# Performance work log

Measured on AMD Instinct MI355X. Metric: run time of the kernel, lower is better.

Reference implementation:

```python
import jax, jax.numpy as jnp
import numpy as np

D_MODEL = 512
NUM_HEADS = 8
D_K = D_MODEL // NUM_HEADS


def setup_inputs() -> dict:
    key = jax.random.key(0)
    ks = jax.random.split(key, 9)
    B, N = 4, 2048
    x = jax.random.normal(ks[0], (B, N, D_MODEL), dtype=jnp.float32)
    s = 1.0 / np.sqrt(D_MODEL)
    Wq = jax.random.normal(ks[1], (D_MODEL, D_MODEL), dtype=jnp.float32) * s
    bq = jax.random.normal(ks[2], (D_MODEL,), dtype=jnp.float32) * 0.02
    Wk = jax.random.normal(ks[3], (D_MODEL, D_MODEL), dtype=jnp.float32) * s
    bk = jax.random.normal(ks[4], (D_MODEL,), dtype=jnp.float32) * 0.02
    Wv = jax.random.normal(ks[5], (D_MODEL, D_MODEL), dtype=jnp.float32) * s
    bv = jax.random.normal(ks[6], (D_MODEL,), dtype=jnp.float32) * 0.02
    Wo = jax.random.normal(ks[7], (D_MODEL, D_MODEL), dtype=jnp.float32) * s
    bo = jax.random.normal(ks[8], (D_MODEL,), dtype=jnp.float32) * 0.02
    return {"x": x, "Wq": Wq, "bq": bq, "Wk": Wk, "bk": bk,
            "Wv": Wv, "bv": bv, "Wo": Wo, "bo": bo}


def reference(x, Wq, bq, Wk, bk, Wv, bv, Wo, bo):
    B, N, _ = x.shape
    # project and split heads: [B, H, N, d_k]
    def split_heads(t):
        return t.reshape(B, N, NUM_HEADS, D_K).transpose(0, 2, 1, 3)
    Q = split_heads(x @ Wq + bq)
    K = split_heads(x @ Wk + bk)
    V = split_heads(x @ Wv + bv)
    scale = 1.0 / np.sqrt(D_K)
    scores = jnp.einsum('bhqd,bhkd->bhqk', Q, K) * scale  # [B,H,N,N]
    probs = jax.nn.softmax(scores, axis=-1)
    attn = jnp.einsum('bhqk,bhkd->bhqd', probs, V)
    attn = attn.transpose(0, 2, 1, 3).reshape(B, N, D_MODEL)
    return attn @ Wo + bo
```

## Files before the change

kernel.cpp:

```cpp
#include <hip/hip_runtime.h>
#include <math.h>

#define D_MODEL 512
#define N_SEQ   2048
#define H       8
#define DK      64

typedef __attribute__((ext_vector_type(8))) short bf16x8;
typedef __attribute__((ext_vector_type(4))) float f32x4;

__device__ __forceinline__ unsigned short f2b(float f) {
    unsigned int u = __float_as_uint(f);
    u += 0x7FFF + ((u >> 16) & 1);
    return (unsigned short)(u >> 16);
}

__global__ void convert_bf16(const float* __restrict__ in,
                             unsigned short* __restrict__ out)
{
    const int i = (blockIdx.x * 256 + threadIdx.x) * 8;
    float4 a = *(const float4*)(in + i);
    float4 b = *(const float4*)(in + i + 4);
    ushort4 o0, o1;
    o0.x = f2b(a.x); o0.y = f2b(a.y); o0.z = f2b(a.z); o0.w = f2b(a.w);
    o1.x = f2b(b.x); o1.y = f2b(b.y); o1.z = f2b(b.z); o1.w = f2b(b.w);
    *(ushort4*)(out + i)     = o0;
    *(ushort4*)(out + i + 4) = o1;
}

__global__ void transpose_all(
    const float* __restrict__ W0, const float* __restrict__ W1,
    const float* __restrict__ W2, const float* __restrict__ W3,
    unsigned short* __restrict__ T0, unsigned short* __restrict__ T1,
    unsigned short* __restrict__ T2, unsigned short* __restrict__ T3)
{
    const float* W; unsigned short* Wt;
    if      (blockIdx.z == 0) { W = W0; Wt = T0; }
    else if (blockIdx.z == 1) { W = W1; Wt = T1; }
    else if (blockIdx.z == 2) { W = W2; Wt = T2; }
    else                      { W = W3; Wt = T3; }

    __shared__ float t[32][33];
    const int tx = threadIdx.x, ty = threadIdx.y;
    const int x = blockIdx.x * 32 + tx;
    const int y0 = blockIdx.y * 32;
    for (int i = ty; i < 32; i += 8)
        t[i][tx] = W[(size_t)(y0 + i) * D_MODEL + x];
    __syncthreads();
    const int ox = blockIdx.y * 32 + tx;
    const int oy0 = blockIdx.x * 32;
    for (int i = ty; i < 32; i += 8)
        Wt[(size_t)(oy0 + i) * D_MODEL + ox] = f2b(t[tx][i]);
}

__device__ __forceinline__ void gemm_body(
    const unsigned short* __restrict__ A,
    const unsigned short* __restrict__ Wt,
    const float* __restrict__ bias,
    void* __restrict__ out, int mode, int bx, int by)
{
    __shared__ unsigned short As[128][72];
    __shared__ unsigned short Bs[128][72];

    const int tid  = threadIdx.x;
    const int lane = tid & 63, wave = tid >> 6;
    const int m0 = by * 128, n0 = bx * 128;
    const int wm = (wave & 1) * 64, wn = (wave >> 1) * 64;
    const int cn = lane & 15, g = lane >> 4;

    const int srow = tid >> 1;
    const int scol = (tid & 1) * 32;
    const unsigned short* Ag = A  + (size_t)(m0 + srow) * D_MODEL + scol;
    const unsigned short* Bg = Wt + (size_t)(n0 + srow) * D_MODEL + scol;

    f32x4 acc[4][4];
    #pragma unroll
    for (int i = 0; i < 4; ++i)
        #pragma unroll
        for (int j = 0; j < 4; ++j)
            acc[i][j] = (f32x4){0.f, 0.f, 0.f, 0.f};

    for (int k0 = 0; k0 < D_MODEL; k0 += 64) {
        bf16x8 av[4], bv[4];
        #pragma unroll
        for (int q = 0; q < 4; ++q) {
            av[q] = *(const bf16x8*)(Ag + k0 + q * 8);
            bv[q] = *(const bf16x8*)(Bg + k0 + q * 8);
        }
        __syncthreads();
        #pragma unroll
        for (int q = 0; q < 4; ++q) {
            *(bf16x8*)&As[srow][scol + q * 8] = av[q];
            *(bf16x8*)&Bs[srow][scol + q * 8] = bv[q];
        }
        __syncthreads();

        #pragma unroll
        for (int ks = 0; ks < 2; ++ks) {
            bf16x8 af[4], bf[4];
            #pragma unroll
            for (int i = 0; i < 4; ++i)
                af[i] = *(const bf16x8*)&As[wm + i * 16 + cn][ks * 32 + g * 8];
            #pragma unroll
            for (int j = 0; j < 4; ++j)
                bf[j] = *(const bf16x8*)&Bs[wn + j * 16 + cn][ks * 32 + g * 8];
            #pragma unroll
            for (int i = 0; i < 4; ++i)
                #pragma unroll
                for (int j = 0; j < 4; ++j)
                    acc[i][j] = __builtin_amdgcn_mfma_f32_16x16x32_bf16(
                        af[i], bf[j], acc[i][j], 0, 0, 0);
        }
    }

    if (mode == 2) {
        float* o = (float*)out;
        #pragma unroll
        for (int j = 0; j < 4; ++j) {
            const int n = n0 + wn + j * 16 + cn;
            const float bb = bias[n];
            #pragma unroll
            for (int i = 0; i < 4; ++i)
                #pragma unroll
                for (int r = 0; r < 4; ++r) {
                    const int m = m0 + wm + i * 16 + g * 4 + r;
                    o[(size_t)m * D_MODEL + n] = acc[i][j][r] + bb;
                }
        }
    } else if (mode == 0) {
        unsigned short* o = (unsigned short*)out;
        #pragma unroll
        for (int j = 0; j < 4; ++j) {
            const int n = n0 + wn + j * 16 + cn;
            const int h = n >> 6, d = n & 63;
            const float bb = bias[n];
            #pragma unroll
            for (int i = 0; i < 4; ++i)
                #pragma unroll
                for (int r = 0; r < 4; ++r) {
                    const int m = m0 + wm + i * 16 + g * 4 + r;
                    const int b = m >> 11, t = m & (N_SEQ - 1);
                    o[(((size_t)b * H + h) * N_SEQ + t) * DK + d] =
                        f2b(acc[i][j][r] + bb);
                }
        }
    } else {
        unsigned short* o = (unsigned short*)out;
        #pragma unroll
        for (int j = 0; j < 4; ++j) {
            const int n = n0 + wn + j * 16 + cn;
            const int h = n >> 6, d = n & 63;
            const float bb = bias[n];
            #pragma unroll
            for (int i = 0; i < 4; ++i) {
                const int m = m0 + wm + i * 16 + g * 4;
                const int b = m >> 11, t = m & (N_SEQ - 1);
                ushort4 pk;
                pk.x = f2b(acc[i][j][0] + bb);
                pk.y = f2b(acc[i][j][1] + bb);
                pk.z = f2b(acc[i][j][2] + bb);
                pk.w = f2b(acc[i][j][3] + bb);
                *(ushort4*)(o + (((size_t)b * H + h) * DK + d) * N_SEQ + t) = pk;
            }
        }
    }
}

__global__ __launch_bounds__(256) void gemm_qkv(
    const unsigned short* __restrict__ A,
    const unsigned short* __restrict__ Wtq,
    const unsigned short* __restrict__ Wtk,
    const unsigned short* __restrict__ Wtv,
    const float* __restrict__ bq, const float* __restrict__ bk,
    const float* __restrict__ bv,
    unsigned short* __restrict__ Qb, unsigned short* __restrict__ Kb,
    unsigned short* __restrict__ Vtb)
{
    const unsigned short* Wt; const float* bias; void* out; int mode;
    if (blockIdx.z == 0)      { Wt = Wtq; bias = bq; out = Qb;  mode = 0; }
    else if (blockIdx.z == 1) { Wt = Wtk; bias = bk; out = Kb;  mode = 0; }
    else                      { Wt = Wtv; bias = bv; out = Vtb; mode = 1; }
    gemm_body(A, Wt, bias, out, mode, blockIdx.x, blockIdx.y);
}

__global__ __launch_bounds__(256) void gemm_o(
    const unsigned short* __restrict__ A,
    const unsigned short* __restrict__ Wt,
    const float* __restrict__ bias, float* __restrict__ out)
{
    gemm_body(A, Wt, bias, out, 2, blockIdx.x, blockIdx.y);
}

__global__ __launch_bounds__(256) void attn_mfma(
    const unsigned short* __restrict__ Q,
    const unsigned short* __restrict__ K,
    const unsigned short* __restrict__ Vt,
    unsigned short* __restrict__ ctx)
{
    __shared__ unsigned short Ks[64][72];
    __shared__ unsigned short Vs[64][72];
    __shared__ unsigned short Ps[4][16][72];

    const int tid = threadIdx.x, lane = tid & 63, wave = tid >> 6;
    const int q0 = blockIdx.x * 64, h = blockIdx.y, b = blockIdx.z;
    const int cn = lane & 15, g = lane >> 4;

    const size_t hb = (size_t)b * H + h;
    const unsigned short* Qp = Q  + hb * N_SEQ * DK;
    const unsigned short* Kp = K  + hb * N_SEQ * DK;
    const unsigned short* Vp = Vt + hb * DK * N_SEQ;

    const int qrow = q0 + wave * 16 + cn;
    bf16x8 bq0 = *(const bf16x8*)(Qp + (size_t)qrow * DK + g * 8);
    bf16x8 bq1 = *(const bf16x8*)(Qp + (size_t)qrow * DK + 32 + g * 8);

    f32x4 O[5];
    #pragma unroll
    for (int i = 0; i < 5; ++i) O[i] = (f32x4){0.f, 0.f, 0.f, 0.f};
    float m_i = -1e30f;

    bf16x8 onesB;
    {
        const short v = (cn == 0) ? (short)0x3F80 : (short)0;
        #pragma unroll
        for (int j = 0; j < 8; ++j) onesB[j] = v;
    }

    const int krow = tid >> 2, kcol = (tid & 3) * 16;
    const float SC = 0.125f;

    for (int j0 = 0; j0 < N_SEQ; j0 += 64) {
        bf16x8 kv0 = *(const bf16x8*)(Kp + (size_t)(j0 + krow) * DK + kcol);
        bf16x8 kv1 = *(const bf16x8*)(Kp + (size_t)(j0 + krow) * DK + kcol + 8);
        bf16x8 vv0 = *(const bf16x8*)(Vp + (size_t)krow * N_SEQ + j0 + kcol);
        bf16x8 vv1 = *(const bf16x8*)(Vp + (size_t)krow * N_SEQ + j0 + kcol + 8);
        __syncthreads();
        *(bf16x8*)&Ks[krow][kcol]     = kv0;
        *(bf16x8*)&Ks[krow][kcol + 8] = kv1;
        *(bf16x8*)&Vs[krow][kcol]     = vv0;
        *(bf16x8*)&Vs[krow][kcol + 8] = vv1;
        __syncthreads();

        f32x4 s[4];
        #pragma unroll
        for (int jt = 0; jt < 4; ++jt) {
            bf16x8 ak0 = *(const bf16x8*)&Ks[jt * 16 + cn][g * 8];
            bf16x8 ak1 = *(const bf16x8*)&Ks[jt * 16 + cn][32 + g * 8];
            f32x4 z = (f32x4){0.f, 0.f, 0.f, 0.f};
            z = __builtin_amdgcn_mfma_f32_16x16x32_bf16(ak0, bq0, z, 0, 0, 0);
            z = __builtin_amdgcn_mfma_f32_16x16x32_bf16(ak1, bq1, z, 0, 0, 0);
            s[jt] = z;
        }

        float mx = s[0][0];
        #pragma unroll
        for (int jt = 0; jt < 4; ++jt)
            #pragma unroll
            for (int r = 0; r < 4; ++r) mx = fmaxf(mx, s[jt][r]);
        mx = fmaxf(mx, __shfl_xor(mx, 16));
        mx = fmaxf(mx, __shfl_xor(mx, 32));
        const float mn = fmaxf(m_i, mx * SC);
        const float alpha = __expf(m_i - mn);
        m_i = mn;

        #pragma unroll
        for (int jt = 0; jt < 4; ++jt) {
            ushort4 pk;
            pk.x = f2b(__expf(fmaf(s[jt][0], SC, -mn)));
            pk.y = f2b(__expf(fmaf(s[jt][1], SC, -mn)));
            pk.z = f2b(__expf(fmaf(s[jt][2], SC, -mn)));
            pk.w = f2b(__expf(fmaf(s[jt][3], SC, -mn)));
            *(ushort4*)&Ps[wave][cn][jt * 16 + g * 4] = pk;
        }

        float al[4];
        #pragma unroll
        for (int r = 0; r < 4; ++r) al[r] = __shfl(alpha, g * 4 + r);
        #pragma unroll
        for (int t = 0; t < 5; ++t)
            #pragma unroll
            for (int r = 0; r < 4; ++r) O[t][r] *= al[r];

        bf16x8 ap0 = *(const bf16x8*)&Ps[wave][cn][g * 8];
        bf16x8 ap1 = *(const bf16x8*)&Ps[wave][cn][32 + g * 8];
        #pragma unroll
        for (int dt = 0; dt < 4; ++dt) {
            bf16x8 bv0 = *(const bf16x8*)&Vs[dt * 16 + cn][g * 8];
            bf16x8 bv1 = *(const bf16x8*)&Vs[dt * 16 + cn][32 + g * 8];
            O[dt] = __builtin_amdgcn_mfma_f32_16x16x32_bf16(ap0, bv0, O[dt], 0, 0, 0);
            O[dt] = __builtin_amdgcn_mfma_f32_16x16x32_bf16(ap1, bv1, O[dt], 0, 0, 0);
        }
        O[4] = __builtin_amdgcn_mfma_f32_16x16x32_bf16(ap0, onesB, O[4], 0, 0, 0);
        O[4] = __builtin_amdgcn_mfma_f32_16x16x32_bf16(ap1, onesB, O[4], 0, 0, 0);
    }

    unsigned short* ob = ctx + (size_t)b * N_SEQ * D_MODEL + (size_t)h * DK;
    #pragma unroll
    for (int r = 0; r < 4; ++r) {
        const float linv = 1.0f / __shfl(O[4][r], g * 16);
        const int q = q0 + wave * 16 + g * 4 + r;
        #pragma unroll
        for (int dt = 0; dt < 4; ++dt)
            ob[(size_t)q * D_MODEL + dt * 16 + cn] = f2b(O[dt][r] * linv);
    }
}

extern "C" void kernel_launch(void* const* d_in, const int* in_sizes, int n_in,
                              void* d_out, int out_size, void* d_ws, size_t ws_size,
                              hipStream_t stream)
{
    const float* x  = (const float*)d_in[0];
    const float* Wq = (const float*)d_in[1];
    const float* bq = (const float*)d_in[2];
    const float* Wk = (const float*)d_in[3];
    const float* bk = (const float*)d_in[4];
    const float* Wv = (const float*)d_in[5];
    const float* bv = (const float*)d_in[6];
    const float* Wo = (const float*)d_in[7];
    const float* bo = (const float*)d_in[8];
    float* out = (float*)d_out;

    const int M = in_sizes[0] / D_MODEL;
    const int B = M / N_SEQ;
    const size_t NX = (size_t)M * D_MODEL;
    const size_t NW = (size_t)D_MODEL * D_MODEL;

    unsigned short* xb  = (unsigned short*)d_ws;
    unsigned short* Wtq = xb  + NX;
    unsigned short* Wtk = Wtq + NW;
    unsigned short* Wtv = Wtk + NW;
    unsigned short* Wto = Wtv + NW;
    unsigned short* Qb  = Wto + NW;
    unsigned short* Kb  = Qb + NX;
    unsigned short* Vtb = Kb + NX;
    unsigned short* ctx = Vtb + NX;

    convert_bf16<<<NX / (256 * 8), 256, 0, stream>>>(x, xb);
    transpose_all<<<dim3(16, 16, 4), dim3(32, 8), 0, stream>>>(
        Wq, Wk, Wv, Wo, Wtq, Wtk, Wtv, Wto);

    gemm_qkv<<<dim3(D_MODEL / 128, M / 128, 3), 256, 0, stream>>>(
        xb, Wtq, Wtk, Wtv, bq, bk, bv, Qb, Kb, Vtb);
    attn_mfma<<<dim3(N_SEQ / 64, H, B), 256, 0, stream>>>(Qb, Kb, Vtb, ctx);
    gemm_o<<<dim3(D_MODEL / 128, M / 128), 256, 0, stream>>>(ctx, Wto, bo, out);
}
```

Baseline: 206.7 us.

## Switch attention to 32x32x16 MFMA with 128-query blocks and exp2 softmax

Rewrites the attention kernel so each wave handles 32 queries using 32x32x16 bf16 MFMA tiles instead of 16x16x32, and each block covers 128 queries. This doubles K/V reuse per LDS load and halves the grid. The softmax now uses exp2 with a pre-scaled log2e factor and packed bf16 conversion. The output is staged through LDS so ctx is written in coalesced 16-byte stores. The cost is more accumulator registers and fewer blocks, which can lower occupancy.

```diff
diff --git a/kernel.cpp b/kernel.cpp
--- a/kernel.cpp
+++ b/kernel.cpp
@@ -6,13 +6,33 @@
 #define H       8
 #define DK      64
 
-typedef __attribute__((ext_vector_type(8))) short bf16x8;
-typedef __attribute__((ext_vector_type(4))) float f32x4;
+typedef __attribute__((ext_vector_type(8)))  short bf16x8;
+typedef __attribute__((ext_vector_type(4)))  float f32x4;
+typedef __attribute__((ext_vector_type(16))) float f32x16;
 
 __device__ __forceinline__ unsigned short f2b(float f) {
     unsigned int u = __float_as_uint(f);
     u += 0x7FFF + ((u >> 16) & 1);
     return (unsigned short)(u >> 16);
+}
+
+__device__ __forceinline__ unsigned int pack2(float lo, float hi) {
+#if __has_builtin(__builtin_amdgcn_cvt_pk_bf16_f32)
+    typedef __attribute__((ext_vector_type(2))) short bf16x2;
+    bf16x2 p = __builtin_amdgcn_cvt_pk_bf16_f32(lo, hi);
+    return (unsigned int)(unsigned short)p[0] |
+           ((unsigned int)(unsigned short)p[1] << 16);
+#else
+    return (unsigned int)f2b(lo) | ((unsigned int)f2b(hi) << 16);
+#endif
+}
+
+__device__ __forceinline__ float fexp2(float x) {
+#if __has_builtin(__builtin_amdgcn_exp2f)
+    return __builtin_amdgcn_exp2f(x);
+#else
+    return __expf(x * 0.6931471805599453f);
+#endif
 }
 
 __global__ void convert_bf16(const float* __restrict__ in,
@@ -199,35 +219,39 @@
 {
     __shared__ unsigned short Ks[64][72];
     __shared__ unsigned short Vs[64][72];
-    __shared__ unsigned short Ps[4][16][72];
+    __shared__ unsigned short Ps[4][32][72];
 
     const int tid = threadIdx.x, lane = tid & 63, wave = tid >> 6;
-    const int q0 = blockIdx.x * 64, h = blockIdx.y, b = blockIdx.z;
-    const int cn = lane & 15, g = lane >> 4;
+    const int q0 = blockIdx.x * 128, h = blockIdx.y, b = blockIdx.z;
+    const int lq = lane & 31;
+    const int hf = lane >> 5;
 
     const size_t hb = (size_t)b * H + h;
     const unsigned short* Qp = Q  + hb * N_SEQ * DK;
     const unsigned short* Kp = K  + hb * N_SEQ * DK;
     const unsigned short* Vp = Vt + hb * DK * N_SEQ;
 
-    const int qrow = q0 + wave * 16 + cn;
-    bf16x8 bq0 = *(const bf16x8*)(Qp + (size_t)qrow * DK + g * 8);
-    bf16x8 bq1 = *(const bf16x8*)(Qp + (size_t)qrow * DK + 32 + g * 8);
-
-    f32x4 O[5];
-    #pragma unroll
-    for (int i = 0; i < 5; ++i) O[i] = (f32x4){0.f, 0.f, 0.f, 0.f};
+    const int qs = q0 + wave * 32;
+
+    bf16x8 qf[4];
+    #pragma unroll
+    for (int kd = 0; kd < 4; ++kd)
+        qf[kd] = *(const bf16x8*)(Qp + (size_t)(qs + lq) * DK + kd * 16 + hf * 8);
+
+    f32x16 O[2], Ol;
+    #pragma unroll
+    for (int r = 0; r < 16; ++r) { O[0][r] = 0.f; O[1][r] = 0.f; Ol[r] = 0.f; }
     float m_i = -1e30f;
 
-    bf16x8 onesB;
+    bf16x8 onesA;
     {
-        const short v = (cn == 0) ? (short)0x3F80 : (short)0;
-        #pragma unroll
-        for (int j = 0; j < 8; ++j) onesB[j] = v;
+        const short v = (lq == 0) ? (short)0x3F80 : (short)0;
+        #pragma unroll
+        for (int j = 0; j < 8; ++j) onesA[j] = v;
     }
 
     const int krow = tid >> 2, kcol = (tid & 3) * 16;
-    const float SC = 0.125f;
+    const float SC2 = 0.18033688011112042f;
 
     for (int j0 = 0; j0 < N_SEQ; j0 += 64) {
         bf16x8 kv0 = *(const bf16x8*)(Kp + (size_t)(j0 + krow) * DK + kcol);
@@ -241,67 +265,76 @@
         *(bf16x8*)&Vs[krow][kcol + 8] = vv1;
         __syncthreads();
 
-        f32x4 s[4];
-        #pragma unroll
-        for (int jt = 0; jt < 4; ++jt) {
-            bf16x8 ak0 = *(const bf16x8*)&Ks[jt * 16 + cn][g * 8];
-            bf16x8 ak1 = *(const bf16x8*)&Ks[jt * 16 + cn][32 + g * 8];
-            f32x4 z = (f32x4){0.f, 0.f, 0.f, 0.f};
-            z = __builtin_amdgcn_mfma_f32_16x16x32_bf16(ak0, bq0, z, 0, 0, 0);
-            z = __builtin_amdgcn_mfma_f32_16x16x32_bf16(ak1, bq1, z, 0, 0, 0);
-            s[jt] = z;
-        }
-
-        float mx = s[0][0];
-        #pragma unroll
-        for (int jt = 0; jt < 4; ++jt)
-            #pragma unroll
-            for (int r = 0; r < 4; ++r) mx = fmaxf(mx, s[jt][r]);
-        mx = fmaxf(mx, __shfl_xor(mx, 16));
+        f32x16 s0, s1;
+        #pragma unroll
+        for (int r = 0; r < 16; ++r) { s0[r] = 0.f; s1[r] = 0.f; }
+        #pragma unroll
+        for (int kd = 0; kd < 4; ++kd) {
+            bf16x8 a0 = *(const bf16x8*)&Ks[lq][kd * 16 + hf * 8];
+            bf16x8 a1 = *(const bf16x8*)&Ks[32 + lq][kd * 16 + hf * 8];
+            s0 = __builtin_amdgcn_mfma_f32_32x32x16_bf16(a0, qf[kd], s0, 0, 0, 0);
+            s1 = __builtin_amdgcn_mfma_f32_32x32x16_bf16(a1, qf[kd], s1, 0, 0, 0);
+        }
+
+        float mx = s0[0];
+        #pragma unroll
+        for (int r = 1; r < 16; ++r) mx = fmaxf(mx, s0[r]);
+        #pragma unroll
+        for (int r = 0; r < 16; ++r) mx = fmaxf(mx, s1[r]);
         mx = fmaxf(mx, __shfl_xor(mx, 32));
-        const float mn = fmaxf(m_i, mx * SC);
-        const float alpha = __expf(m_i - mn);
+        const float mn = fmaxf(m_i, mx * SC2);
+        const float alpha = fexp2(m_i - mn);
         m_i = mn;
 
-        #pragma unroll
-        for (int jt = 0; jt < 4; ++jt) {
-            ushort4 pk;
-            pk.x = f2b(__expf(fmaf(s[jt][0], SC, -mn)));
-            pk.y = f2b(__expf(fmaf(s[jt][1], SC, -mn)));
-            pk.z = f2b(__expf(fmaf(s[jt][2], SC, -mn)));
-            pk.w = f2b(__expf(fmaf(s[jt][3], SC, -mn)));
-            *(ushort4*)&Ps[wave][cn][jt * 16 + g * 4] = pk;
-        }
-
-        float al[4];
-        #pragma unroll
-        for (int r = 0; r < 4; ++r) al[r] = __shfl(alpha, g * 4 + r);
-        #pragma unroll
-        for (int t = 0; t < 5; ++t)
-            #pragma unroll
-            for (int r = 0; r < 4; ++r) O[t][r] *= al[r];
-
-        bf16x8 ap0 = *(const bf16x8*)&Ps[wave][cn][g * 8];
-        bf16x8 ap1 = *(const bf16x8*)&Ps[wave][cn][32 + g * 8];
-        #pragma unroll
-        for (int dt = 0; dt < 4; ++dt) {
-            bf16x8 bv0 = *(const bf16x8*)&Vs[dt * 16 + cn][g * 8];
-            bf16x8 bv1 = *(const bf16x8*)&Vs[dt * 16 + cn][32 + g * 8];
-            O[dt] = __builtin_amdgcn_mfma_f32_16x16x32_bf16(ap0, bv0, O[dt], 0, 0, 0);
-            O[dt] = __builtin_amdgcn_mfma_f32_16x16x32_bf16(ap1, bv1, O[dt], 0, 0, 0);
-        }
-        O[4] = __builtin_amdgcn_mfma_f32_16x16x32_bf16(ap0, onesB, O[4], 0, 0, 0);
-        O[4] = __builtin_amdgcn_mfma_f32_16x16x32_bf16(ap1, onesB, O[4], 0, 0, 0);
-    }
-
-    unsigned short* ob = ctx + (size_t)b * N_SEQ * D_MODEL + (size_t)h * DK;
-    #pragma unroll
-    for (int r = 0; r < 4; ++r) {
-        const float linv = 1.0f / __shfl(O[4][r], g * 16);
-        const int q = q0 + wave * 16 + g * 4 + r;
-        #pragma unroll
-        for (int dt = 0; dt < 4; ++dt)
-            ob[(size_t)q * D_MODEL + dt * 16 + cn] = f2b(O[dt][r] * linv);
+        unsigned int* prow = (unsigned int*)&Ps[wave][lq][0];
+        #pragma unroll
+        for (int j = 0; j < 8; ++j) {
+            const float p0 = fexp2(fmaf(s0[2 * j],     SC2, -mn));
+            const float p1 = fexp2(fmaf(s0[2 * j + 1], SC2, -mn));
+            prow[(j & 1) + 4 * (j >> 1) + 2 * hf] = pack2(p0, p1);
+        }
+        #pragma unroll
+        for (int j = 0; j < 8; ++j) {
+            const float p0 = fexp2(fmaf(s1[2 * j],     SC2, -mn));
+            const float p1 = fexp2(fmaf(s1[2 * j + 1], SC2, -mn));
+            prow[16 + (j & 1) + 4 * (j >> 1) + 2 * hf] = pack2(p0, p1);
+        }
+
+        #pragma unroll
+        for (int r = 0; r < 16; ++r) {
+            O[0][r] *= alpha; O[1][r] *= alpha; Ol[r] *= alpha;
+        }
+
+        #pragma unroll
+        for (int ks = 0; ks < 4; ++ks) {
+            bf16x8 bp = *(const bf16x8*)&Ps[wave][lq][ks * 16 + hf * 8];
+            bf16x8 a0 = *(const bf16x8*)&Vs[lq][ks * 16 + hf * 8];
+            bf16x8 a1 = *(const bf16x8*)&Vs[32 + lq][ks * 16 + hf * 8];
+            O[0] = __builtin_amdgcn_mfma_f32_32x32x16_bf16(a0, bp, O[0], 0, 0, 0);
+            O[1] = __builtin_amdgcn_mfma_f32_32x32x16_bf16(a1, bp, O[1], 0, 0, 0);
+            Ol   = __builtin_amdgcn_mfma_f32_32x32x16_bf16(onesA, bp, Ol, 0, 0, 0);
+        }
+    }
+
+    const float linv = 1.0f / __shfl(Ol[0], lq);
+
+    unsigned int* prow = (unsigned int*)&Ps[wave][lq][0];
+    #pragma unroll
+    for (int dt = 0; dt < 2; ++dt)
+        #pragma unroll
+        for (int rp = 0; rp < 8; ++rp) {
+            const float v0 = O[dt][2 * rp]     * linv;
+            const float v1 = O[dt][2 * rp + 1] * linv;
+            prow[16 * dt + (rp & 1) + 4 * (rp >> 1) + 2 * hf] = pack2(v0, v1);
+        }
+
+    const int rr = lane >> 1, hh = lane & 1;
+    unsigned short* ob = ctx + ((size_t)b * N_SEQ + (q0 + wave * 32 + rr)) * D_MODEL
+                             + h * DK + hh * 32;
+    #pragma unroll
+    for (int t = 0; t < 4; ++t) {
+        bf16x8 v = *(const bf16x8*)&Ps[wave][rr][hh * 32 + t * 8];
+        *(bf16x8*)(ob + t * 8) = v;
     }
 }
 
@@ -341,6 +374,6 @@
 
     gemm_qkv<<<dim3(D_MODEL / 128, M / 128, 3), 256, 0, stream>>>(
         xb, Wtq, Wtk, Wtv, bq, bk, bv, Qb, Kb, Vtb);
-    attn_mfma<<<dim3(N_SEQ / 64, H, B), 256, 0, stream>>>(Qb, Kb, Vtb, ctx);
+    attn_mfma<<<dim3(N_SEQ / 128, H, B), 256, 0, stream>>>(Qb, Kb, Vtb, ctx);
     gemm_o<<<dim3(D_MODEL / 128, M / 128), 256, 0, stream>>>(ctx, Wto, bo, out);
 }
```

New measurement: 201.6 us. -2.5%, faster.
